# Kernel tuning notes

Measured on AMD Instinct MI355X. Metric: run time of the kernel, lower is better.

The kernel has to match this reference:

```python
import jax, jax.numpy as jnp
import numpy as np
import math

E = 250000          # number of edges
N = 25000           # number of nodes
R_MAX = 4.0         # radial cutoff (data['r_max'])
NUM_NEIGHBORS = 3.8 # self.num_neighbors
NUM_BASIS = 3       # FullyConnectedNet([3, 256, ...])
# irrep slices of the l=0..3 spherical-harmonic feature vector: (start, stop, 2l+1)
SLICES = ((0, 1, 1.0), (1, 4, 3.0), (4, 9, 5.0), (9, 16, 7.0))


def _sph_l3(v):
    """e3nn real spherical harmonics l=0..3, 'component' normalization, unit input. [E,3]->[E,16]"""
    x, y, z = v[:, 0], v[:, 1], v[:, 2]
    x2, y2, z2 = x * x, y * y, z * z
    s3, s5, s7, s15, s105 = math.sqrt(3.), math.sqrt(5.), math.sqrt(7.), math.sqrt(15.), math.sqrt(105.)
    c358, c218 = math.sqrt(35. / 8.), math.sqrt(21. / 8.)
    sh = [jnp.ones_like(x),
          s3 * x, s3 * y, s3 * z,
          s15 * x * z, s15 * x * y, 0.5 * s5 * (2. * y2 - x2 - z2), s15 * y * z, 0.5 * s15 * (z2 - x2),
          c358 * x * (3. * z2 - x2), s105 * x * y * z, c218 * x * (4. * y2 - z2 - x2),
          0.5 * s7 * y * (2. * y2 - 3. * z2 - 3. * x2), c218 * z * (4. * y2 - z2 - x2),
          0.5 * s105 * y * (z2 - x2), c358 * z * (z2 - 3. * x2)]
    return jnp.stack(sh, axis=-1)


def _radial_basis(edge_len):
    # soft_one_hot_linspace(.., basis='gaussian', cutoff=False), 3 bins on [0, R_MAX]
    centers = jnp.linspace(0.0, R_MAX, NUM_BASIS)
    step = centers[1] - centers[0]
    d = (edge_len[:, None] - centers) / step
    return jnp.exp(-d * d) / 1.12  # [E,3]


def _mlp(s, Wa, Wb):
    # FullyConnectedNet([3,256,out]) with relu: x @ W / sqrt(fan_in) per layer
    h = jax.nn.relu(s @ Wa / math.sqrt(float(NUM_BASIS)))
    return h @ Wb / math.sqrt(256.0)


def _forward(edge_vec, edge_len, W1a, W1b, W2a, W2b, edge_src, edge_dst):
    v = edge_vec / (jnp.linalg.norm(edge_vec, axis=-1, keepdims=True) + 1e-12)
    sh = _sph_l3(v)                               # [E,16] edge_attr
    basis = _radial_basis(edge_len)               # [E,3]  edge_scalars
    inv_nn = 1.0 / math.sqrt(NUM_NEIGHBORS)

    # initial node features: scatter of edge_attr
    x = jax.ops.segment_sum(sh, edge_dst, num_segments=N) * inv_nn   # [N,16]

    # conv1: gather + fully-connected TP (l x l -> 0 paths) + scatter
    w1 = _mlp(basis, W1a, W1b).reshape(-1, 4, 96)  # [E,4,96] per-path weights
    xs = x[edge_src]                               # [E,16] gather
    dots = jnp.stack([(xs[:, a:b] * sh[:, a:b]).sum(-1) / math.sqrt(d)
                      for a, b, d in SLICES], axis=-1)   # [E,4] CG l x l -> 0
    ef = jnp.einsum('ep,epk->ek', dots, w1) * 0.5  # /sqrt(4 paths), [E,96]
    h = jax.ops.segment_sum(ef, edge_dst, num_segments=N) * inv_nn   # [N,96]

    # gate: 32 scalars (relu/abs), 32 gates (relu/tanh alternating), 32 gated
    s, g, vv = h[:, :32], h[:, 32:64], h[:, 64:96]
    s_act = jnp.concatenate([jax.nn.relu(s[:, :16]), jnp.abs(s[:, 16:])], -1)
    g_act = jnp.concatenate([jax.nn.relu(g[:, :8]), jnp.tanh(g[:, 8:16]),
                             jax.nn.relu(g[:, 16:24]), jnp.tanh(g[:, 24:])], -1)
    y = jnp.concatenate([s_act, g_act * vv], -1)   # [N,64]

    w2 = _mlp(basis, W2a, W2b)                     # [E,64]
    ef2 = (y[edge_src] * w2).sum(-1, keepdims=True) / 8.0  # /sqrt(64)
    return jax.ops.segment_sum(ef2, edge_dst, num_segments=N) * inv_nn  # [N,1]


def setup_inputs() -> dict:
    key = jax.random.key(0)
    ks = jax.random.split(key, 8)
    return {
        'edge_vec': jax.random.normal(ks[0], (E, 3), jnp.float32),
        'edge_len': jax.random.uniform(ks[1], (E,), jnp.float32, 0.5, R_MAX),
        'W1a': jax.random.normal(ks[2], (NUM_BASIS, 256), jnp.float32),
        'W1b': jax.random.normal(ks[3], (256, 4 * 96), jnp.float32),
        'W2a': jax.random.normal(ks[4], (NUM_BASIS, 256), jnp.float32),
        'W2b': jax.random.normal(ks[5], (256, 64), jnp.float32),
        'edge_src': jax.random.randint(ks[6], (E,), 0, N),
        'edge_dst': jax.random.randint(ks[7], (E,), 0, N),
    }


def reference(edge_vec, edge_len, W1a, W1b, W2a, W2b, edge_src, edge_dst):
    return _forward(edge_vec, edge_len, W1a, W1b, W2a, W2b, edge_src, edge_dst)
```

## Files before the change

### kernel.cpp

```cpp
#include <hip/hip_runtime.h>
#include <math.h>

#define BPB 4
#define CAP 64
static const int LBINS = 1024;

__device__ __forceinline__ unsigned short f2bf(float f) {
    unsigned int u = __float_as_uint(f);
    unsigned int r = (u + 0x7FFFu + ((u >> 16) & 1u)) >> 16;
    return (unsigned short)r;
}
__device__ __forceinline__ unsigned int packbf(float lo, float hi) {
    return (unsigned int)f2bf(lo) | ((unsigned int)f2bf(hi) << 16);
}
__device__ __forceinline__ float bflo(unsigned int u) { return __uint_as_float(u << 16); }
__device__ __forceinline__ float bfhi(unsigned int u) { return __uint_as_float(u & 0xFFFF0000u); }

__device__ __forceinline__ void sph_l3(float x, float y, float z, float* sh) {
    const float s3   = 1.7320508075688772f;
    const float s5   = 2.23606797749979f;
    const float s7   = 2.6457513110645906f;
    const float s15  = 3.872983346207417f;
    const float s105 = 10.246950765959598f;
    const float c358 = 2.0916500663351889f;
    const float c218 = 1.6201851746019651f;
    float x2 = x * x, y2 = y * y, z2 = z * z;
    sh[0]  = 1.0f;
    sh[1]  = s3 * x;
    sh[2]  = s3 * y;
    sh[3]  = s3 * z;
    sh[4]  = s15 * x * z;
    sh[5]  = s15 * x * y;
    sh[6]  = 0.5f * s5 * (2.0f * y2 - x2 - z2);
    sh[7]  = s15 * y * z;
    sh[8]  = 0.5f * s15 * (z2 - x2);
    sh[9]  = c358 * x * (3.0f * z2 - x2);
    sh[10] = s105 * x * y * z;
    sh[11] = c218 * x * (4.0f * y2 - z2 - x2);
    sh[12] = 0.5f * s7 * y * (2.0f * y2 - 3.0f * z2 - 3.0f * x2);
    sh[13] = c218 * z * (4.0f * y2 - z2 - x2);
    sh[14] = 0.5f * s105 * y * (z2 - x2);
    sh[15] = c358 * z * (z2 - 3.0f * x2);
}

template<int STR>
__device__ __forceinline__ void gemmB(const float* __restrict__ col,
                                      const float (*__restrict__ hs)[256], float* acc) {
#pragma unroll 8
    for (int cc = 0; cc < 256; ++cc) {
        float w = col[(size_t)cc * STR];
#pragma unroll
        for (int b = 0; b < BPB; ++b) acc[b] += hs[b][cc] * w;
    }
}

__global__ __launch_bounds__(256) void k_table(const float* __restrict__ W1a,
                                               const float* __restrict__ W1b,
                                               const float* __restrict__ W2a,
                                               const float* __restrict__ W2b,
                                               unsigned int* __restrict__ T1,
                                               unsigned int* __restrict__ T2, int lbins,
                                               int* __restrict__ cursor, int N) {
    __shared__ float h1s[BPB][256];
    __shared__ float h2s[BPB][256];
    const int c = threadIdx.x;
    const int bin0 = blockIdx.x * BPB;
    const int half = blockIdx.y;

    if (half == 0) {
        int zi = blockIdx.x * 256 + c;
        if (zi < N) cursor[zi] = 0;
    }

    const float inv_s3 = 0.57735026918962576f;
    const float bin2len = 4.0f / (float)(lbins - 1);
    float w1a0 = W1a[c], w1a1 = W1a[256 + c], w1a2 = W1a[512 + c];
    float w2a0 = W2a[c], w2a1 = W2a[256 + c], w2a2 = W2a[512 + c];
#pragma unroll
    for (int b = 0; b < BPB; ++b) {
        float len = (float)(bin0 + b) * bin2len;
        float d0 = len * 0.5f;
        float d1 = (len - 2.0f) * 0.5f;
        float d2 = (len - 4.0f) * 0.5f;
        float b0 = expf(-d0 * d0) * (1.0f / 1.12f);
        float b1 = expf(-d1 * d1) * (1.0f / 1.12f);
        float b2 = expf(-d2 * d2) * (1.0f / 1.12f);
        h1s[b][c] = fmaxf((b0 * w1a0 + b1 * w1a1 + b2 * w1a2) * inv_s3, 0.0f);
        if (half == 1)
            h2s[b][c] = fmaxf((b0 * w2a0 + b1 * w2a1 + b2 * w2a2) * inv_s3, 0.0f);
    }
    __syncthreads();

    float acc[BPB];
#pragma unroll
    for (int b = 0; b < BPB; ++b) acc[b] = 0.0f;
    int o = -1;
    if (half == 0) {
        if (c < 224) { o = c; gemmB<384>(W1b + o, h1s, acc); }
    } else {
        if (c < 64)       { o = 384 + c; gemmB<64>(W2b + c, h2s, acc); }
        else if (c < 224) { o = 160 + c; gemmB<384>(W1b + (160 + c), h1s, acc); }
    }
    if (o >= 0) {
        unsigned short* Ts1 = (unsigned short*)T1;
        unsigned short* Ts2 = (unsigned short*)T2;
        if (o < 384) {
            int k = o % 96, pp = o / 96;
#pragma unroll
            for (int b = 0; b < BPB; ++b) {
                int i = bin0 + b;
                unsigned short hv = f2bf(acc[b] * (1.0f / 16.0f));
                Ts1[(((size_t)i * 96 + k) * 4 + pp) * 2] = hv;
                if (i > 0) Ts1[(((size_t)(i - 1) * 96 + k) * 4 + pp) * 2 + 1] = hv;
            }
        } else {
            int k2 = o - 384;
#pragma unroll
            for (int b = 0; b < BPB; ++b) {
                int i = bin0 + b;
                unsigned short hv = f2bf(acc[b] * (1.0f / 16.0f));
                Ts2[((size_t)i * 64 + k2) * 2] = hv;
                if (i > 0) Ts2[((size_t)(i - 1) * 64 + k2) * 2 + 1] = hv;
            }
        }
    }
}

__global__ void k_scatter(const float* __restrict__ evec, const float* __restrict__ elen,
                          const int* __restrict__ esrc, const int* __restrict__ edst,
                          int* __restrict__ cursor,
                          uint4* __restrict__ shB4, uint2* __restrict__ edgeSL,
                          int E, int lbins) {
    int e = blockIdx.x * blockDim.x + threadIdx.x;
    if (e >= E) return;
    int d = edst[e];
    int slotIdx = atomicAdd(&cursor[d], 1);
    if (slotIdx >= CAP) return;
    size_t pos = ((size_t)d << 6) + slotIdx;

    float vx = evec[3 * e], vy = evec[3 * e + 1], vz = evec[3 * e + 2];
    float nrm = sqrtf(vx * vx + vy * vy + vz * vz);
    float inv = 1.0f / (nrm + 1e-12f);
    float sh[16];
    sph_l3(vx * inv, vy * inv, vz * inv, sh);
    uint4 a, b;
    a.x = packbf(sh[0], sh[1]);  a.y = packbf(sh[2], sh[3]);
    a.z = packbf(sh[4], sh[5]);  a.w = packbf(sh[6], sh[7]);
    b.x = packbf(sh[8], sh[9]);  b.y = packbf(sh[10], sh[11]);
    b.z = packbf(sh[12], sh[13]); b.w = packbf(sh[14], sh[15]);
    shB4[pos * 2]     = a;
    shB4[pos * 2 + 1] = b;

    float len = elen[e];
    float p = fminf(fmaxf(len, 0.0f), 4.0f) * ((float)(lbins - 1) / 4.0f);
    if (p > (float)(lbins - 1) - 1.0f) p = (float)(lbins - 1) - 1.0f;
    edgeSL[pos] = make_uint2((unsigned int)esrc[e], __float_as_uint(p));
}

__device__ __forceinline__ void unpack16(uint4 a, uint4 b, float* s) {
    s[0] = bflo(a.x);  s[1] = bfhi(a.x);  s[2] = bflo(a.y);  s[3] = bfhi(a.y);
    s[4] = bflo(a.z);  s[5] = bfhi(a.z);  s[6] = bflo(a.w);  s[7] = bfhi(a.w);
    s[8] = bflo(b.x);  s[9] = bfhi(b.x);  s[10] = bflo(b.y); s[11] = bfhi(b.y);
    s[12] = bflo(b.z); s[13] = bfhi(b.z); s[14] = bflo(b.w); s[15] = bfhi(b.w);
}

__global__ void k_x(const uint4* __restrict__ shB4, const int* __restrict__ cursor,
                    float4* __restrict__ x4, int N) {
    int n = blockIdx.x * blockDim.x + threadIdx.x;
    if (n >= N) return;
    float acc[16];
#pragma unroll
    for (int i = 0; i < 16; ++i) acc[i] = 0.0f;
    int cnt = min(cursor[n], CAP);
    size_t base = (size_t)n << 6;
    for (int j = 0; j < cnt; ++j) {
        uint4 a = shB4[(base + j) * 2], b = shB4[(base + j) * 2 + 1];
        float s[16];
        unpack16(a, b, s);
#pragma unroll
        for (int i = 0; i < 16; ++i) acc[i] += s[i];
    }
    const float inv_nn = 0.51298917604257706f;
    float4* xp = x4 + (size_t)n * 4;
    xp[0] = make_float4(acc[0] * inv_nn, acc[1] * inv_nn, acc[2] * inv_nn, acc[3] * inv_nn);
    xp[1] = make_float4(acc[4] * inv_nn, acc[5] * inv_nn, acc[6] * inv_nn, acc[7] * inv_nn);
    xp[2] = make_float4(acc[8] * inv_nn, acc[9] * inv_nn, acc[10] * inv_nn, acc[11] * inv_nn);
    xp[3] = make_float4(acc[12] * inv_nn, acc[13] * inv_nn, acc[14] * inv_nn, acc[15] * inv_nn);
}

__global__ __launch_bounds__(128) void k_hy(const uint4* __restrict__ shB4,
                                            const uint2* __restrict__ edgeSL,
                                            const int* __restrict__ cursor,
                                            const float4* __restrict__ x4,
                                            const unsigned int* __restrict__ T1,
                                            float* __restrict__ y, int N) {
    int n = blockIdx.x;
    if (n >= N) return;
    int kk = threadIdx.x;
    __shared__ float4 sdots[CAP];
    __shared__ float spos[CAP];
    __shared__ float hs[96];
    int cnt = min(cursor[n], CAP);
    size_t base = (size_t)n << 6;
    const float rs3 = 0.57735026918962576f;
    const float rs5 = 0.44721359549995793f;
    const float rs7 = 0.37796447300922720f;

    if (kk < cnt) {
        size_t j = base + kk;
        uint2 sl = edgeSL[j];
        uint4 a = shB4[j * 2], b = shB4[j * 2 + 1];
        float s[16];
        unpack16(a, b, s);
        const float4* xr = x4 + (size_t)sl.x * 4;
        float4 x0 = xr[0], x1 = xr[1], x2 = xr[2], x3 = xr[3];
        float d0 = x0.x * s[0];
        float d1 = x0.y * s[1] + x0.z * s[2] + x0.w * s[3];
        float d2 = x1.x * s[4] + x1.y * s[5] + x1.z * s[6] + x1.w * s[7] + x2.x * s[8];
        float d3 = x2.y * s[9] + x2.z * s[10] + x2.w * s[11]
                 + x3.x * s[12] + x3.y * s[13] + x3.z * s[14] + x3.w * s[15];
        sdots[kk] = make_float4(d0, d1 * rs3, d2 * rs5, d3 * rs7);
        spos[kk] = __uint_as_float(sl.y);
    }
    __syncthreads();
    if (kk < 96) {
        float acc = 0.0f;
        for (int q = 0; q < cnt; ++q) {
            float4 dt = sdots[q];
            float p = spos[q];
            int i0 = (int)p;
            float f = p - (float)i0;
            uint4 u = *(const uint4*)(T1 + ((((size_t)i0 * 96) + kk) << 2));
            float a0 = bflo(u.x), b0 = bfhi(u.x);
            float a1 = bflo(u.y), b1 = bfhi(u.y);
            float a2 = bflo(u.z), b2 = bfhi(u.z);
            float a3 = bflo(u.w), b3 = bfhi(u.w);
            acc += dt.x * (a0 + f * (b0 - a0)) + dt.y * (a1 + f * (b1 - a1))
                 + dt.z * (a2 + f * (b2 - a2)) + dt.w * (a3 + f * (b3 - a3));
        }
        const float scale = 0.25649458802128853f;
        hs[kk] = acc * scale;
    }
    __syncthreads();
    int t = threadIdx.x;
    if (t < 64) {
        float outv;
        if (t < 32) {
            float v = hs[t];
            outv = (t < 16) ? fmaxf(v, 0.0f) : fabsf(v);
        } else {
            int kg = t - 32;
            float g = hs[32 + kg];
            float vv = hs[64 + kg];
            float ga = (kg < 8 || (kg >= 16 && kg < 24)) ? fmaxf(g, 0.0f) : tanhf(g);
            outv = ga * vv;
        }
        y[(size_t)n * 64 + t] = outv;
    }
}

__global__ void k_out(const uint2* __restrict__ edgeSL, const int* __restrict__ cursor,
                      const float* __restrict__ y,
                      const unsigned int* __restrict__ T2, float* __restrict__ out, int N) {
    int n = (blockIdx.x * blockDim.x + threadIdx.x) >> 6;
    int lane = threadIdx.x & 63;
    if (n >= N) return;
    int cnt = min(cursor[n], CAP);
    size_t base = (size_t)n << 6;
    float acc = 0.0f;
    for (int j = 0; j < cnt; ++j) {
        uint2 sl = edgeSL[base + j];
        float p = __uint_as_float(sl.y);
        int i0 = (int)p;
        float f = p - (float)i0;
        unsigned int u = T2[(size_t)i0 * 64 + lane];
        float w0 = bflo(u), w1 = bfhi(u);
        float w2v = w0 + f * (w1 - w0);
        acc += y[(size_t)sl.x * 64 + lane] * w2v;
    }
#pragma unroll
    for (int off = 32; off > 0; off >>= 1) acc += __shfl_xor(acc, off, 64);
    if (lane == 0) out[n] = acc * (0.51298917604257706f / 8.0f);
}

extern "C" void kernel_launch(void* const* d_in, const int* in_sizes, int n_in,
                              void* d_out, int out_size, void* d_ws, size_t ws_size,
                              hipStream_t stream) {
    const float* evec = (const float*)d_in[0];
    const float* elen = (const float*)d_in[1];
    const float* W1a  = (const float*)d_in[2];
    const float* W1b  = (const float*)d_in[3];
    const float* W2a  = (const float*)d_in[4];
    const float* W2b  = (const float*)d_in[5];
    const int* esrc   = (const int*)d_in[6];
    const int* edst   = (const int*)d_in[7];
    const int E = in_sizes[1];
    const int N = out_size;
    float* out = (float*)d_out;

    char* ws = (char*)d_ws;
    size_t off = 0;
    auto alloc = [&](size_t bytes) -> void* {
        void* p = ws + off;
        off = (off + bytes + 255) & ~(size_t)255;
        return p;
    };

    int*    cursor = (int*)alloc((size_t)N * 4);
    uint4*  shB4   = (uint4*)alloc((size_t)N * CAP * 32);
    uint2*  edgeSL = (uint2*)alloc((size_t)N * CAP * 8);
    float4* x4     = (float4*)alloc((size_t)N * 64);
    float*  y      = (float*)alloc((size_t)N * 64 * 4);

    int lbins = LBINS;
    if (ws_size > off) {
        size_t avail = ws_size - off;
        size_t maxbins = avail / (96 * 16 + 64 * 4);
        if ((size_t)lbins > maxbins) lbins = (int)((maxbins / BPB) * BPB);
    }
    if (lbins < 2 * BPB) lbins = 2 * BPB;
    unsigned int* T1 = (unsigned int*)alloc((size_t)lbins * 96 * 16);
    unsigned int* T2 = (unsigned int*)alloc((size_t)lbins * 64 * 4);

    k_table<<<dim3(lbins / BPB, 2), 256, 0, stream>>>(W1a, W1b, W2a, W2b, T1, T2, lbins,
                                                      cursor, N);
    k_scatter<<<(E + 255) / 256, 256, 0, stream>>>(evec, elen, esrc, edst, cursor,
                                                   shB4, edgeSL, E, lbins);
    k_x<<<(N + 255) / 256, 256, 0, stream>>>(shB4, cursor, x4, N);
    k_hy<<<N, 128, 0, stream>>>(shB4, edgeSL, cursor, x4, T1, y, N);
    {
        long long threads = (long long)N * 64;
        int blocks = (int)((threads + 255) / 256);
        k_out<<<blocks, 256, 0, stream>>>(edgeSL, cursor, y, T2, out, N);
    }
}
```

Baseline: 106.1 us.

## Use wavefront-per-node mapping in k_x and pack four nodes per k_hy block

k_x switches from one thread per node with a serial edge loop to one 64-lane wavefront per node, where each lane loads one edge and the 16-component sum is done with cross-lane shuffles. k_hy goes from one 128-thread block per node (with 32 idle threads in the table stage) to 256-thread blocks holding four nodes, one wavefront each. Each lane now handles one output channel plus a second one for the first 32 lanes. Small unroll pragmas are added to the edge loops. The aim is more memory parallelism and fewer idle threads and blocks, at the cost of many shuffles in k_x and uneven per-lane work in k_hy.

New measurement: 116.3 us. +9.6%, slower.

```diff
diff --git a/kernel.cpp b/kernel.cpp
--- a/kernel.cpp
+++ b/kernel.cpp
@@ -43,6 +43,13 @@
     sh[15] = c358 * z * (z2 - 3.0f * x2);
 }
 
+__device__ __forceinline__ void unpack16(uint4 a, uint4 b, float* s) {
+    s[0] = bflo(a.x);  s[1] = bfhi(a.x);  s[2] = bflo(a.y);  s[3] = bfhi(a.y);
+    s[4] = bflo(a.z);  s[5] = bfhi(a.z);  s[6] = bflo(a.w);  s[7] = bfhi(a.w);
+    s[8] = bflo(b.x);  s[9] = bfhi(b.x);  s[10] = bflo(b.y); s[11] = bfhi(b.y);
+    s[12] = bflo(b.z); s[13] = bfhi(b.z); s[14] = bflo(b.w); s[15] = bfhi(b.w);
+}
+
 template<int STR>
 __device__ __forceinline__ void gemmB(const float* __restrict__ col,
                                       const float (*__restrict__ hs)[256], float* acc) {
@@ -157,57 +164,58 @@
     edgeSL[pos] = make_uint2((unsigned int)esrc[e], __float_as_uint(p));
 }
 
-__device__ __forceinline__ void unpack16(uint4 a, uint4 b, float* s) {
-    s[0] = bflo(a.x);  s[1] = bfhi(a.x);  s[2] = bflo(a.y);  s[3] = bfhi(a.y);
-    s[4] = bflo(a.z);  s[5] = bfhi(a.z);  s[6] = bflo(a.w);  s[7] = bfhi(a.w);
-    s[8] = bflo(b.x);  s[9] = bfhi(b.x);  s[10] = bflo(b.y); s[11] = bfhi(b.y);
-    s[12] = bflo(b.z); s[13] = bfhi(b.z); s[14] = bflo(b.w); s[15] = bfhi(b.w);
-}
-
-__global__ void k_x(const uint4* __restrict__ shB4, const int* __restrict__ cursor,
-                    float4* __restrict__ x4, int N) {
-    int n = blockIdx.x * blockDim.x + threadIdx.x;
+__global__ __launch_bounds__(256) void k_x(const uint4* __restrict__ shB4,
+                                           const int* __restrict__ cursor,
+                                           float4* __restrict__ x4, int N) {
+    int n = (blockIdx.x * blockDim.x + threadIdx.x) >> 6;
+    int lane = threadIdx.x & 63;
     if (n >= N) return;
-    float acc[16];
-#pragma unroll
-    for (int i = 0; i < 16; ++i) acc[i] = 0.0f;
     int cnt = min(cursor[n], CAP);
-    size_t base = (size_t)n << 6;
-    for (int j = 0; j < cnt; ++j) {
-        uint4 a = shB4[(base + j) * 2], b = shB4[(base + j) * 2 + 1];
-        float s[16];
+    float s[16];
+    if (lane < cnt) {
+        size_t j = ((size_t)n << 6) + lane;
+        uint4 a = shB4[j * 2], b = shB4[j * 2 + 1];
         unpack16(a, b, s);
-#pragma unroll
-        for (int i = 0; i < 16; ++i) acc[i] += s[i];
-    }
-    const float inv_nn = 0.51298917604257706f;
-    float4* xp = x4 + (size_t)n * 4;
-    xp[0] = make_float4(acc[0] * inv_nn, acc[1] * inv_nn, acc[2] * inv_nn, acc[3] * inv_nn);
-    xp[1] = make_float4(acc[4] * inv_nn, acc[5] * inv_nn, acc[6] * inv_nn, acc[7] * inv_nn);
-    xp[2] = make_float4(acc[8] * inv_nn, acc[9] * inv_nn, acc[10] * inv_nn, acc[11] * inv_nn);
-    xp[3] = make_float4(acc[12] * inv_nn, acc[13] * inv_nn, acc[14] * inv_nn, acc[15] * inv_nn);
-}
-
-__global__ __launch_bounds__(128) void k_hy(const uint4* __restrict__ shB4,
+    } else {
+#pragma unroll
+        for (int i = 0; i < 16; ++i) s[i] = 0.0f;
+    }
+#pragma unroll
+    for (int off = 32; off > 0; off >>= 1) {
+#pragma unroll
+        for (int i = 0; i < 16; ++i) s[i] += __shfl_xor(s[i], off, 64);
+    }
+    if (lane == 0) {
+        const float inv_nn = 0.51298917604257706f;
+        float4* xp = x4 + (size_t)n * 4;
+        xp[0] = make_float4(s[0] * inv_nn, s[1] * inv_nn, s[2] * inv_nn, s[3] * inv_nn);
+        xp[1] = make_float4(s[4] * inv_nn, s[5] * inv_nn, s[6] * inv_nn, s[7] * inv_nn);
+        xp[2] = make_float4(s[8] * inv_nn, s[9] * inv_nn, s[10] * inv_nn, s[11] * inv_nn);
+        xp[3] = make_float4(s[12] * inv_nn, s[13] * inv_nn, s[14] * inv_nn, s[15] * inv_nn);
+    }
+}
+
+__global__ __launch_bounds__(256) void k_hy(const uint4* __restrict__ shB4,
                                             const uint2* __restrict__ edgeSL,
                                             const int* __restrict__ cursor,
                                             const float4* __restrict__ x4,
                                             const unsigned int* __restrict__ T1,
                                             float* __restrict__ y, int N) {
-    int n = blockIdx.x;
-    if (n >= N) return;
-    int kk = threadIdx.x;
-    __shared__ float4 sdots[CAP];
-    __shared__ float spos[CAP];
-    __shared__ float hs[96];
-    int cnt = min(cursor[n], CAP);
+    const int w = threadIdx.x >> 6;
+    const int lane = threadIdx.x & 63;
+    const int n = blockIdx.x * 4 + w;
+    const bool valid = n < N;
+    __shared__ float4 sdots[4][CAP];
+    __shared__ float spos[4][CAP];
+    __shared__ float hs[4][96];
+    int cnt = valid ? min(cursor[n], CAP) : 0;
     size_t base = (size_t)n << 6;
     const float rs3 = 0.57735026918962576f;
     const float rs5 = 0.44721359549995793f;
     const float rs7 = 0.37796447300922720f;
 
-    if (kk < cnt) {
-        size_t j = base + kk;
+    if (lane < cnt) {
+        size_t j = base + lane;
         uint2 sl = edgeSL[j];
         uint4 a = shB4[j * 2], b = shB4[j * 2 + 1];
         float s[16];
@@ -219,43 +227,56 @@
         float d2 = x1.x * s[4] + x1.y * s[5] + x1.z * s[6] + x1.w * s[7] + x2.x * s[8];
         float d3 = x2.y * s[9] + x2.z * s[10] + x2.w * s[11]
                  + x3.x * s[12] + x3.y * s[13] + x3.z * s[14] + x3.w * s[15];
-        sdots[kk] = make_float4(d0, d1 * rs3, d2 * rs5, d3 * rs7);
-        spos[kk] = __uint_as_float(sl.y);
+        sdots[w][lane] = make_float4(d0, d1 * rs3, d2 * rs5, d3 * rs7);
+        spos[w][lane] = __uint_as_float(sl.y);
     }
     __syncthreads();
-    if (kk < 96) {
-        float acc = 0.0f;
-        for (int q = 0; q < cnt; ++q) {
-            float4 dt = sdots[q];
-            float p = spos[q];
-            int i0 = (int)p;
-            float f = p - (float)i0;
-            uint4 u = *(const uint4*)(T1 + ((((size_t)i0 * 96) + kk) << 2));
+
+    float acc0 = 0.0f, acc1 = 0.0f;
+#pragma unroll 2
+    for (int q = 0; q < cnt; ++q) {
+        float4 dt = sdots[w][q];
+        float p = spos[w][q];
+        int i0 = (int)p;
+        float f = p - (float)i0;
+        const unsigned int* row = T1 + ((size_t)i0 * 96 << 2);
+        uint4 u = *(const uint4*)(row + (lane << 2));
+        {
             float a0 = bflo(u.x), b0 = bfhi(u.x);
             float a1 = bflo(u.y), b1 = bfhi(u.y);
             float a2 = bflo(u.z), b2 = bfhi(u.z);
             float a3 = bflo(u.w), b3 = bfhi(u.w);
-            acc += dt.x * (a0 + f * (b0 - a0)) + dt.y * (a1 + f * (b1 - a1))
-                 + dt.z * (a2 + f * (b2 - a2)) + dt.w * (a3 + f * (b3 - a3));
+            acc0 += dt.x * (a0 + f * (b0 - a0)) + dt.y * (a1 + f * (b1 - a1))
+                  + dt.z * (a2 + f * (b2 - a2)) + dt.w * (a3 + f * (b3 - a3));
         }
-        const float scale = 0.25649458802128853f;
-        hs[kk] = acc * scale;
-    }
+        if (lane < 32) {
+            uint4 v = *(const uint4*)(row + ((64 + lane) << 2));
+            float a0 = bflo(v.x), b0 = bfhi(v.x);
+            float a1 = bflo(v.y), b1 = bfhi(v.y);
+            float a2 = bflo(v.z), b2 = bfhi(v.z);
+            float a3 = bflo(v.w), b3 = bfhi(v.w);
+            acc1 += dt.x * (a0 + f * (b0 - a0)) + dt.y * (a1 + f * (b1 - a1))
+                  + dt.z * (a2 + f * (b2 - a2)) + dt.w * (a3 + f * (b3 - a3));
+        }
+    }
+    const float scale = 0.25649458802128853f;
+    hs[w][lane] = acc0 * scale;
+    if (lane < 32) hs[w][64 + lane] = acc1 * scale;
     __syncthreads();
-    int t = threadIdx.x;
-    if (t < 64) {
+
+    if (valid) {
         float outv;
-        if (t < 32) {
-            float v = hs[t];
-            outv = (t < 16) ? fmaxf(v, 0.0f) : fabsf(v);
+        if (lane < 32) {
+            float v = hs[w][lane];
+            outv = (lane < 16) ? fmaxf(v, 0.0f) : fabsf(v);
         } else {
-            int kg = t - 32;
-            float g = hs[32 + kg];
-            float vv = hs[64 + kg];
+            int kg = lane - 32;
+            float g = hs[w][32 + kg];
+            float vv = hs[w][64 + kg];
             float ga = (kg < 8 || (kg >= 16 && kg < 24)) ? fmaxf(g, 0.0f) : tanhf(g);
             outv = ga * vv;
         }
-        y[(size_t)n * 64 + t] = outv;
+        y[(size_t)n * 64 + lane] = outv;
     }
 }
 
@@ -268,6 +289,7 @@
     int cnt = min(cursor[n], CAP);
     size_t base = (size_t)n << 6;
     float acc = 0.0f;
+#pragma unroll 2
     for (int j = 0; j < cnt; ++j) {
         uint2 sl = edgeSL[base + j];
         float p = __uint_as_float(sl.y);
@@ -326,8 +348,12 @@
                                                       cursor, N);
     k_scatter<<<(E + 255) / 256, 256, 0, stream>>>(evec, elen, esrc, edst, cursor,
                                                    shB4, edgeSL, E, lbins);
-    k_x<<<(N + 255) / 256, 256, 0, stream>>>(shB4, cursor, x4, N);
-    k_hy<<<N, 128, 0, stream>>>(shB4, edgeSL, cursor, x4, T1, y, N);
+    {
+        long long threads = (long long)N * 64;
+        int blocks = (int)((threads + 255) / 256);
+        k_x<<<blocks, 256, 0, stream>>>(shB4, cursor, x4, N);
+    }
+    k_hy<<<(N + 3) / 4, 256, 0, stream>>>(shB4, edgeSL, cursor, x4, T1, y, N);
     {
         long long threads = (long long)N * 64;
         int blocks = (int)((threads + 255) / 256);
```
